# Kernel optimization log

Hardware: AMD Instinct MI355X
Metric: run time of the kernel (lower is better)

Reference implementation:

```python
import jax, jax.numpy as jnp
import numpy as np
import math

D_MODEL = 512
N_HEADS = 8
K_NEIGHBORS = 30
B, S = 4, 2048
N_VARIATES = 8
EPS = 1e-5


def layer_norm(x, g, b):
    m = jnp.mean(x, axis=-1, keepdims=True)
    v = jnp.mean(jnp.square(x - m), axis=-1, keepdims=True)
    return (x - m) * jax.lax.rsqrt(v + EPS) * g + b


def mha(x, mask, w_in, b_in, w_out, b_out):
    # x: [B,S,D]; mask: [B,S,S] bool, True = blocked (same for every head)
    Bb, Ss, D = x.shape
    H, dh = N_HEADS, D // N_HEADS
    qkv = x @ w_in.T + b_in                      # [B,S,3D]
    q, k, v = jnp.split(qkv, 3, axis=-1)
    q = q.reshape(Bb, Ss, H, dh).transpose(0, 2, 1, 3)
    k = k.reshape(Bb, Ss, H, dh).transpose(0, 2, 1, 3)
    v = v.reshape(Bb, Ss, H, dh).transpose(0, 2, 1, 3)
    scores = jnp.einsum('bhqd,bhkd->bhqk', q, k) / math.sqrt(dh)
    scores = jnp.where(mask[:, None, :, :], -jnp.inf, scores)
    attn = jax.nn.softmax(scores, axis=-1)
    o = jnp.einsum('bhqk,bhkd->bhqd', attn, v)
    o = o.transpose(0, 2, 1, 3).reshape(Bb, Ss, D)
    return o @ w_out.T + b_out


def build_masks(variates, times, valid_mask):
    Bb, Ss = variates.shape
    eye = jnp.eye(Ss, dtype=bool)
    same_var = variates[:, :, None] == variates[:, None, :]      # [B,S,S]
    valid_2d = valid_mask[:, :, None] & valid_mask[:, None, :]
    intra_mask = ~(same_var & valid_2d)                          # True = blocked
    blocked_i = jnp.any(jnp.all(intra_mask, axis=-1))
    intra_mask = intra_mask & ~(blocked_i & eye)                 # unblock diagonal if any row fully blocked

    diff_var = ~same_var
    time_dist = jnp.abs(times[:, :, None] - times[:, None, :])
    time_dist = jnp.where(~valid_2d | ~diff_var, jnp.inf, time_dist)
    k = min(K_NEIGHBORS, Ss)
    _, topk_idx = jax.lax.top_k(-time_dist, k)                   # k smallest distances
    b_idx = jnp.arange(Bb)[:, None, None]
    r_idx = jnp.arange(Ss)[None, :, None]
    knn_mask = jnp.zeros((Bb, Ss, Ss), dtype=bool).at[b_idx, r_idx, topk_idx].set(True)
    knn_mask = knn_mask & valid_2d
    inter_mask = ~knn_mask
    blocked_e = jnp.any(jnp.all(inter_mask, axis=-1))
    inter_mask = inter_mask & ~(blocked_e & eye)
    return intra_mask, inter_mask


def setup_inputs() -> dict:
    key = jax.random.key(0)
    ks = jax.random.split(key, 12)
    D = D_MODEL
    s = 0.02
    inp = {
        'x': jax.random.normal(ks[0], (B, S, D), dtype=jnp.float32),
        'variates': jax.random.randint(ks[1], (B, S), 0, N_VARIATES),
        'times': jax.random.uniform(ks[2], (B, S), dtype=jnp.float32),
        'valid_mask': jnp.ones((B, S), dtype=bool),
        'in_w1': jax.random.normal(ks[3], (3 * D, D), dtype=jnp.float32) * s,
        'in_b1': jnp.zeros((3 * D,), dtype=jnp.float32),
        'out_w1': jax.random.normal(ks[4], (D, D), dtype=jnp.float32) * s,
        'out_b1': jnp.zeros((D,), dtype=jnp.float32),
        'ln_g1': jnp.ones((D,), dtype=jnp.float32),
        'ln_b1': jnp.zeros((D,), dtype=jnp.float32),
        'in_w2': jax.random.normal(ks[5], (3 * D, D), dtype=jnp.float32) * s,
        'in_b2': jnp.zeros((3 * D,), dtype=jnp.float32),
        'out_w2': jax.random.normal(ks[6], (D, D), dtype=jnp.float32) * s,
        'out_b2': jnp.zeros((D,), dtype=jnp.float32),
        'ln_g2': jnp.ones((D,), dtype=jnp.float32),
        'ln_b2': jnp.zeros((D,), dtype=jnp.float32),
    }
    return inp


def reference(x, variates, times, valid_mask,
              in_w1, in_b1, out_w1, out_b1, ln_g1, ln_b1,
              in_w2, in_b2, out_w2, out_b2, ln_g2, ln_b2):
    intra_mask, inter_mask = build_masks(variates, times, valid_mask)
    a1 = mha(x, intra_mask, in_w1, in_b1, out_w1, out_b1)
    x = layer_norm(x + a1, ln_g1, ln_b1)
    a2 = mha(x, inter_mask, in_w2, in_b2, out_w2, out_b2)
    x = layer_norm(x + a2, ln_g2, ln_b2)
    return x
```

## Files before the change

kernel.cpp:

```cpp
#include <hip/hip_runtime.h>


#define S_LEN 2048
#define BATCH 4
#define DM    512
#define NH    8
#define DH    64
#define KNN_K 30
#define NVAR  8
#define NTOK  (BATCH * S_LEN)
#define QKVD  (3 * DM)
#define PADCAP 2560
#define MAXTILE 40

typedef float f32x4 __attribute__((ext_vector_type(4)));
typedef short s16x8 __attribute__((ext_vector_type(8)));
typedef short s16x4 __attribute__((ext_vector_type(4)));

__device__ __forceinline__ float bf2f(short u) {
  return __uint_as_float(((unsigned)(unsigned short)u) << 16);
}
__device__ __forceinline__ short f2bf(float f) {
  unsigned x = __float_as_uint(f);
  return (short)((x + 0x7fffu + ((x >> 16) & 1u)) >> 16);
}

#define C_N0 (NTOK * DM / 4)
#define C_N1 (QKVD * DM / 4)
#define C_N2 (DM * DM / 4)
#define C_B1 (C_N0 + C_N1)
#define C_B2 (C_B1 + C_N2)
#define C_B3 (C_B2 + C_N1)
#define C_B4 (C_B3 + C_N2)
#define PREP_GRID (2 * BATCH + C_B4 / 1024)

__global__ __launch_bounds__(1024) void prep_cast(
    const int* __restrict__ variates, const float* __restrict__ times,
    int* __restrict__ gcnt, int* __restrict__ pgoff, int* __restrict__ porig,
    int* __restrict__ tileV, int* __restrict__ tileQ0, int* __restrict__ ntile,
    float* __restrict__ flistT, int* __restrict__ flistI, int* __restrict__ flenG,
    int* __restrict__ sortI,
    const float* __restrict__ s0, const float* __restrict__ s1,
    const float* __restrict__ s2, const float* __restrict__ s3,
    const float* __restrict__ s4, short* __restrict__ d0,
    short* __restrict__ d1, short* __restrict__ d2,
    short* __restrict__ d3, short* __restrict__ d4) {
  int blk = blockIdx.x;
  int tid = threadIdx.x;

  if (blk < BATCH) {
    int b = blk;
    __shared__ unsigned hcnt[2048];
    __shared__ int boff[2049];
    __shared__ float bt[S_LEN];
    __shared__ int bp2[S_LEN];
    __shared__ unsigned wsum[16];
    __shared__ unsigned woff[16];

    hcnt[tid] = 0; hcnt[tid + 1024] = 0;
    float t0 = times[b * S_LEN + tid];
    float t1 = times[b * S_LEN + tid + 1024];
    int p0 = (variates[b * S_LEN + tid] << 12) | tid;
    int p1 = (variates[b * S_LEN + tid + 1024] << 12) | (tid + 1024);
    int k0 = (int)(t0 * 2048.0f); k0 = k0 < 0 ? 0 : (k0 > 2047 ? 2047 : k0);
    int k1 = (int)(t1 * 2048.0f); k1 = k1 < 0 ? 0 : (k1 > 2047 ? 2047 : k1);
    __syncthreads();
    atomicAdd(&hcnt[k0], 1u);
    atomicAdd(&hcnt[k1], 1u);
    __syncthreads();
    int wv = tid >> 6, lane = tid & 63;
    int base = wv * 128 + lane * 2;
    unsigned c0 = hcnt[base], c1 = hcnt[base + 1];
    unsigned s = c0 + c1;
    unsigned inc = s;
#pragma unroll
    for (int o2 = 1; o2 < 64; o2 <<= 1) {
      unsigned tt = __shfl_up(inc, o2);
      if (lane >= o2) inc += tt;
    }
    if (lane == 63) wsum[wv] = inc;
    __syncthreads();
    if (tid == 0) {
      unsigned a = 0;
      for (int w2 = 0; w2 < 16; ++w2) { woff[w2] = a; a += wsum[w2]; }
    }
    __syncthreads();
    unsigned e0 = woff[wv] + (inc - s);
    unsigned e1 = e0 + c0;
    boff[base] = (int)e0; boff[base + 1] = (int)e1;
    hcnt[base] = e0; hcnt[base + 1] = e1;
    if (tid == 0) boff[2048] = S_LEN;
    __syncthreads();
    unsigned q0 = atomicAdd(&hcnt[k0], 1u);
    bt[q0] = t0; bp2[q0] = p0;
    unsigned q1 = atomicAdd(&hcnt[k1], 1u);
    bt[q1] = t1; bp2[q1] = p1;
    __syncthreads();
#pragma unroll
    for (int bk = 0; bk < 2; ++bk) {
      int k = tid + bk * 1024;
      int s2 = boff[k], e2 = boff[k + 1];
      for (int i = s2 + 1; i < e2; ++i) {
        float tv = bt[i]; int pv = bp2[i];
        int j = i - 1;
        while (j >= s2 && (bt[j] > tv ||
               (bt[j] == tv && (bp2[j] & 0xFFF) > (pv & 0xFFF)))) {
          bt[j + 1] = bt[j]; bp2[j + 1] = bp2[j]; --j;
        }
        bt[j + 1] = tv; bp2[j + 1] = pv;
      }
    }
    __syncthreads();
    for (int i = tid; i < S_LEN; i += 1024)
      sortI[b * S_LEN + i] = bp2[i] & 0xFFF;
    if (wv < NVAR) {
      int lbase = lane * 32;
      int c = 0;
#pragma unroll
      for (int i = 0; i < 32; ++i) c += ((bp2[lbase + i] >> 12) != wv) ? 1 : 0;
      int pc = c;
#pragma unroll
      for (int o2 = 1; o2 < 64; o2 <<= 1) {
        int t2 = __shfl_up(pc, o2);
        if (lane >= o2) pc += t2;
      }
      int pos = pc - c;
      size_t fb = (size_t)(b * NVAR + wv) * S_LEN;
      for (int i = 0; i < 32; ++i) {
        int e = bp2[lbase + i];
        if ((e >> 12) != wv) {
          flistT[fb + pos] = bt[lbase + i];
          flistI[fb + pos] = e & 0xFFF;
          ++pos;
        }
      }
      if (lane == 63) flenG[b * NVAR + wv] = pc;
    }
  } else if (blk < 2 * BATCH) {
    int b = blk - BATCH;
    int t = tid;
    __shared__ int scnt[64][NVAR];
    __shared__ int soff[64][NVAR];
    __shared__ int stot[NVAR], sbase[NVAR];
    for (int p = t; p < PADCAP; p += 1024) porig[b * PADCAP + p] = -1;
    const int* vb = variates + b * S_LEN;
    int c[NVAR] = {0, 0, 0, 0, 0, 0, 0, 0};
    if (t < 64) {
      for (int j = t * 32; j < t * 32 + 32; ++j) {
        int v = vb[j];
#pragma unroll
        for (int u = 0; u < NVAR; ++u) c[u] += (v == u);
      }
#pragma unroll
      for (int u = 0; u < NVAR; ++u) scnt[t][u] = c[u];
    }
    __syncthreads();
    if (t < NVAR) {
      int a = 0;
      for (int u = 0; u < 64; ++u) { soff[u][t] = a; a += scnt[u][t]; }
      stot[t] = a;
    }
    __syncthreads();
    if (t == 0) {
      int a = 0, nt = 0;
      for (int v = 0; v < NVAR; ++v) {
        sbase[v] = a;
        pgoff[b * NVAR + v] = a;
        gcnt[b * NVAR + v] = stot[v];
        int ntv = (stot[v] + 63) >> 6;
        for (int i = 0; i < ntv; ++i) {
          tileV[b * MAXTILE + nt] = v;
          tileQ0[b * MAXTILE + nt] = a + i * 64;
          ++nt;
        }
        a += ntv * 64;
      }
      ntile[b] = nt;
    }
    __syncthreads();
    if (t < 64) {
      int o[NVAR];
#pragma unroll
      for (int u = 0; u < NVAR; ++u) o[u] = sbase[u] + soff[t][u];
      for (int j = t * 32; j < t * 32 + 32; ++j) {
        int v = vb[j];
        int dst = 0;
#pragma unroll
        for (int u = 0; u < NVAR; ++u) dst += (v == u) ? o[u] : 0;
        porig[b * PADCAP + dst] = j;
#pragma unroll
        for (int u = 0; u < NVAR; ++u) o[u] += (v == u);
      }
    }
  } else {
    int i = (blk - 2 * BATCH) * 1024 + tid;
    const float* src; short* dst; int k;
    if (i < C_N0)      { src = s0; dst = d0; k = i; }
    else if (i < C_B1) { src = s1; dst = d1; k = i - C_N0; }
    else if (i < C_B2) { src = s2; dst = d2; k = i - C_B1; }
    else if (i < C_B3) { src = s3; dst = d3; k = i - C_B2; }
    else               { src = s4; dst = d4; k = i - C_B3; }
    float4 v = ((const float4*)src)[k];
    s16x4 o;
    o[0] = f2bf(v.x); o[1] = f2bf(v.y); o[2] = f2bf(v.z); o[3] = f2bf(v.w);
    ((s16x4*)dst)[k] = o;
  }
}

__global__ __launch_bounds__(256) void knn_grp(const float* __restrict__ times,
                                               const int* __restrict__ porig,
                                               const int* __restrict__ pgoff,
                                               const int* __restrict__ gcnt,
                                               const float* __restrict__ flistT,
                                               const int* __restrict__ flistI,
                                               const int* __restrict__ flenG,
                                               int* __restrict__ out) {
  __shared__ float ft[S_LEN];
  __shared__ int fi[S_LEN];
  int tid = threadIdx.x;
  int bv = blockIdx.x >> 3;
  int chunk = blockIdx.x & 7;
  int b = bv >> 3, v = bv & 7;
  int flen = flenG[bv];
  size_t fb = (size_t)bv * S_LEN;
  for (int i = tid; i < flen; i += 256) {
    ft[i] = flistT[fb + i];
    fi[i] = flistI[fb + i];
  }
  __syncthreads();

  int cnt = gcnt[b * NVAR + v];
  int off = pgoff[b * NVAR + v];
  int qi = chunk * 256 + tid;
  if (qi >= cnt) return;
  int j = porig[b * PADCAP + off + qi];
  float tq = times[b * S_LEN + j];

  int lo = 0, hi = flen;
  while (lo < hi) {
    int mid = (lo + hi) >> 1;
    if (ft[mid] < tq) lo = mid + 1; else hi = mid;
  }
  int L = lo - 1, R = lo;

  float dt[KNN_K];
  int ti[KNN_K];
#pragma unroll
  for (int i = 0; i < KNN_K; ++i) {
    float dL = (L >= 0) ? (tq - ft[L]) : __builtin_inff();
    float dR = (R < flen) ? (ft[R] - tq) : __builtin_inff();
    if (dL <= dR) { dt[i] = dL; ti[i] = fi[L]; --L; }
    else          { dt[i] = dR; ti[i] = fi[R]; ++R; }
  }
  float tau = dt[KNN_K - 1];
  int nLess = 0;
#pragma unroll
  for (int i = 0; i < KNN_K; ++i) nLess += (dt[i] < tau) ? 1 : 0;

  int* op = out + ((size_t)b * S_LEN + j) * KNN_K;
#pragma unroll
  for (int i = 0; i < KNN_K; ++i)
    if (i < nLess) op[i] = ti[i];

  int m = KNN_K - nLess;
  int last = -1;
  for (int s = 0; s < m; ++s) {
    int best = 0x7fffffff;
#pragma unroll
    for (int i = 0; i < KNN_K; ++i)
      if (dt[i] == tau && ti[i] > last && ti[i] < best) best = ti[i];
    for (int Lw = L; Lw >= 0; --Lw) {
      float d = tq - ft[Lw];
      if (d > tau) break;
      if (d == tau) {
        int ix = fi[Lw];
        if (ix > last && ix < best) best = ix;
      }
    }
    for (int Rw = R; Rw < flen; ++Rw) {
      float d = ft[Rw] - tq;
      if (d > tau) break;
      if (d == tau) {
        int ix = fi[Rw];
        if (ix > last && ix < best) best = ix;
      }
    }
    op[nLess + s] = best;
    last = best;
  }
}

template <int OUT_BF16>
__global__ __launch_bounds__(256) void gemm_bt(const short* __restrict__ A,
                                               const short* __restrict__ Bm,
                                               const float* __restrict__ bias,
                                               void* __restrict__ Cout,
                                               int M, int N, int K) {
  __shared__ short sA[128 * 40];
  __shared__ short sB[128 * 40];
  int n0 = blockIdx.x * 128, m0 = blockIdx.y * 128;
  int tid = threadIdx.x;
  int lane = tid & 63, wv = tid >> 6;
  int wr = wv >> 1, wc = wv & 1;

  int srow = tid >> 2;
  int scol = (tid & 3) * 8;
  const short* aG = A + (size_t)(m0 + srow) * K + scol;
  const short* bG = Bm + (size_t)(n0 + srow) * K + scol;

  f32x4 acc[4][4] = {};
  int nk = K >> 5;

  s16x8 pa0 = *(const s16x8*)(aG);
  s16x8 pa1 = *(const s16x8*)(aG + (size_t)64 * K);
  s16x8 pb0 = *(const s16x8*)(bG);
  s16x8 pb1 = *(const s16x8*)(bG + (size_t)64 * K);

  for (int kt = 0; kt < nk; ++kt) {
    __syncthreads();
    *(s16x8*)&sA[srow * 40 + scol] = pa0;
    *(s16x8*)&sA[(srow + 64) * 40 + scol] = pa1;
    *(s16x8*)&sB[srow * 40 + scol] = pb0;
    *(s16x8*)&sB[(srow + 64) * 40 + scol] = pb1;
    __syncthreads();
    if (kt + 1 < nk) {
      const short* a2 = aG + (kt + 1) * 32;
      const short* b2 = bG + (kt + 1) * 32;
      pa0 = *(const s16x8*)(a2);
      pa1 = *(const s16x8*)(a2 + (size_t)64 * K);
      pb0 = *(const s16x8*)(b2);
      pb1 = *(const s16x8*)(b2 + (size_t)64 * K);
    }
    int kb = (lane >> 4) * 8;
    int ar = wr * 64 + (lane & 15);
    int br = wc * 64 + (lane & 15);
    s16x8 af[4], bf[4];
#pragma unroll
    for (int m = 0; m < 4; ++m) af[m] = *(const s16x8*)&sA[(ar + m * 16) * 40 + kb];
#pragma unroll
    for (int n = 0; n < 4; ++n) bf[n] = *(const s16x8*)&sB[(br + n * 16) * 40 + kb];
#pragma unroll
    for (int m = 0; m < 4; ++m)
#pragma unroll
      for (int n = 0; n < 4; ++n)
        acc[m][n] = __builtin_amdgcn_mfma_f32_16x16x32_bf16(af[m], bf[n], acc[m][n], 0, 0, 0);
  }

  int crow0 = m0 + wr * 64 + ((lane >> 4) * 4);
  int ccol0 = n0 + wc * 64 + (lane & 15);
#pragma unroll
  for (int n = 0; n < 4; ++n) {
    int col = ccol0 + n * 16;
    float bv = bias ? bias[col] : 0.f;
#pragma unroll
    for (int m = 0; m < 4; ++m) {
#pragma unroll
      for (int j = 0; j < 4; ++j) {
        int row = crow0 + m * 16 + j;
        float val = acc[m][n][j] + bv;
        if (OUT_BF16)
          ((short*)Cout)[(size_t)row * N + col] = f2bf(val);
        else
          ((float*)Cout)[(size_t)row * N + col] = val;
      }
    }
  }
}

__global__ __launch_bounds__(256) void intra_attn(
    const short* __restrict__ qkv, const int* __restrict__ porig,
    const int* __restrict__ tileV, const int* __restrict__ tileQ0,
    const int* __restrict__ ntile, const int* __restrict__ pgoff,
    const int* __restrict__ gcnt, short* __restrict__ o) {
  int b = blockIdx.z, h = blockIdx.y, t = blockIdx.x;
  if (t >= ntile[b]) return;
  int v = tileV[b * MAXTILE + t];
  int q0 = tileQ0[b * MAXTILE + t];
  int k0 = pgoff[b * NVAR + v];
  int L = gcnt[b * NVAR + v];
  int nch = (L + 63) >> 6;

  __shared__ short sQ[2][64][40];
  __shared__ short sK[2][64][40];
  __shared__ short sVT[2][64][40];
  __shared__ short sP[2][64][40];

  int tid = threadIdx.x, lane = tid & 63, w = tid >> 6;
  int colbase = lane & 15;
  int kfrag = (lane >> 4) * 8;
  int r = tid >> 2, cc = (tid & 3) * 16;

  {
    int tok = porig[b * PADCAP + q0 + r];
    if (tok < 0) tok = 0;
    const short* src = qkv + ((size_t)(b * S_LEN + tok)) * QKVD + h * DH + cc;
    s16x8 v0 = *(const s16x8*)src;
    s16x8 v1 = *(const s16x8*)(src + 8);
    int half = cc >> 5, kk = cc & 31;
    *(s16x8*)&sQ[half][r][kk] = v0;
    *(s16x8*)&sQ[half][r][kk + 8] = v1;
  }

  s16x8 pk0, pk1, pv0, pv1;
  {
    int tok = porig[b * PADCAP + k0 + r];
    if (tok < 0) tok = 0;
    size_t rowg = (size_t)(b * S_LEN + tok) * QKVD;
    const short* srcK = qkv + rowg + DM + h * DH + cc;
    pk0 = *(const s16x8*)srcK;
    pk1 = *(const s16x8*)(srcK + 8);
    const short* srcV = qkv + rowg + 2 * DM + h * DH + cc;
    pv0 = *(const s16x8*)srcV;
    pv1 = *(const s16x8*)(srcV + 8);
  }

  f32x4 accO[4] = {};
  float lrun[4] = {0.f, 0.f, 0.f, 0.f};

  for (int c = 0; c < nch; ++c) {
    __syncthreads();
    {
      int half = cc >> 5, kk = cc & 31;
      *(s16x8*)&sK[half][r][kk] = pk0;
      *(s16x8*)&sK[half][r][kk + 8] = pk1;
      int khalf = r >> 5, kkv = r & 31;
#pragma unroll
      for (int i = 0; i < 8; ++i) {
        int row = cc + i;
        sVT[khalf][row][kkv ^ (((row >> 4) & 3) << 3)] = pv0[i];
      }
#pragma unroll
      for (int i = 0; i < 8; ++i) {
        int row = cc + 8 + i;
        sVT[khalf][row][kkv ^ (((row >> 4) & 3) << 3)] = pv1[i];
      }
    }
    __syncthreads();
    if (c + 1 < nch) {
      int tok = porig[b * PADCAP + k0 + (c + 1) * 64 + r];
      if (tok < 0) tok = 0;
      size_t rowg = (size_t)(b * S_LEN + tok) * QKVD;
      const short* srcK = qkv + rowg + DM + h * DH + cc;
      pk0 = *(const s16x8*)srcK;
      pk1 = *(const s16x8*)(srcK + 8);
      const short* srcV = qkv + rowg + 2 * DM + h * DH + cc;
      pv0 = *(const s16x8*)srcV;
      pv1 = *(const s16x8*)(srcV + 8);
    }

    s16x8 aQ0 = *(const s16x8*)&sQ[0][w * 16 + colbase][kfrag];
    s16x8 aQ1 = *(const s16x8*)&sQ[1][w * 16 + colbase][kfrag];
    f32x4 accS[4] = {};
#pragma unroll
    for (int n = 0; n < 4; ++n) {
      s16x8 b0 = *(const s16x8*)&sK[0][n * 16 + colbase][kfrag];
      s16x8 b1 = *(const s16x8*)&sK[1][n * 16 + colbase][kfrag];
      accS[n] = __builtin_amdgcn_mfma_f32_16x16x32_bf16(aQ0, b0, accS[n], 0, 0, 0);
      accS[n] = __builtin_amdgcn_mfma_f32_16x16x32_bf16(aQ1, b1, accS[n], 0, 0, 0);
    }

    float pv[4][4];
#pragma unroll
    for (int j = 0; j < 4; ++j) {
      float rs = 0.f;
#pragma unroll
      for (int n = 0; n < 4; ++n) {
        bool ok = (c * 64 + n * 16 + colbase) < L;
        float p = ok ? __expf(accS[n][j] * 0.125f) : 0.f;
        pv[n][j] = p;
        rs += p;
      }
      for (int o2 = 8; o2; o2 >>= 1) rs += __shfl_xor(rs, o2);
      lrun[j] += rs;
    }

    int prow = w * 16 + ((lane >> 4) << 2);
#pragma unroll
    for (int n = 0; n < 4; ++n)
#pragma unroll
      for (int j = 0; j < 4; ++j)
        sP[n >> 1][prow + j][colbase + ((n & 1) << 4)] = f2bf(pv[n][j]);

    s16x8 aP0 = *(const s16x8*)&sP[0][w * 16 + colbase][kfrag];
    s16x8 aP1 = *(const s16x8*)&sP[1][w * 16 + colbase][kfrag];
#pragma unroll
    for (int n = 0; n < 4; ++n) {
      int row = n * 16 + colbase;
      int cb = kfrag ^ ((n & 3) << 3);
      s16x8 b0 = *(const s16x8*)&sVT[0][row][cb];
      s16x8 b1 = *(const s16x8*)&sVT[1][row][cb];
      accO[n] = __builtin_amdgcn_mfma_f32_16x16x32_bf16(aP0, b0, accO[n], 0, 0, 0);
      accO[n] = __builtin_amdgcn_mfma_f32_16x16x32_bf16(aP1, b1, accO[n], 0, 0, 0);
    }
  }

#pragma unroll
  for (int j = 0; j < 4; ++j) {
    int prow = w * 16 + (lane >> 4) * 4 + j;
    int orig = porig[b * PADCAP + q0 + prow];
    if (orig >= 0) {
      float inv = 1.f / lrun[j];
      size_t base = ((size_t)(b * S_LEN + orig)) * DM + h * DH;
#pragma unroll
      for (int n = 0; n < 4; ++n)
        o[base + n * 16 + colbase] = f2bf(accO[n][j] * inv);
    }
  }
}

__global__ __launch_bounds__(256) void inter_attn(const short* __restrict__ qkv,
                                                  const int* __restrict__ knn,
                                                  const int* __restrict__ sortI,
                                                  short* __restrict__ o) {
  __shared__ float sS[4][NH][33];
  __shared__ float sP[4][NH][33];
  int tid = threadIdx.x, lane = tid & 63, w = tid >> 6;
  int rank = blockIdx.x * 4 + w;
  int b = rank >> 11;
  int q = sortI[b * S_LEN + (rank & 2047)];
  int bq = b * S_LEN + q;
  int h = lane >> 3;

  int myidx = (lane < KNN_K) ? knn[(size_t)bq * KNN_K + lane] : 0;

  s16x8 q8 = *(const s16x8*)(qkv + (size_t)bq * QKVD + lane * 8);
  float qf[8];
#pragma unroll
  for (int i = 0; i < 8; ++i) qf[i] = bf2f(q8[i]) * 0.125f;

  for (int j = 0; j < KNN_K; ++j) {
    int idx = __shfl(myidx, j);
    s16x8 k8 = *(const s16x8*)(qkv + ((size_t)(b * S_LEN + idx)) * QKVD + DM + lane * 8);
    float acc = 0.f;
#pragma unroll
    for (int i = 0; i < 8; ++i) acc += qf[i] * bf2f(k8[i]);
    acc += __shfl_xor(acc, 1);
    acc += __shfl_xor(acc, 2);
    acc += __shfl_xor(acc, 4);
    if ((lane & 7) == 0) sS[w][h][j] = acc;
  }

  int jsub = lane & 7;
  float sv0 = sS[w][h][jsub];
  float sv1 = sS[w][h][jsub + 8];
  float sv2 = sS[w][h][jsub + 16];
  float sv3 = (jsub < 6) ? sS[w][h][jsub + 24] : -__builtin_inff();
  float m = fmaxf(fmaxf(sv0, sv1), fmaxf(sv2, sv3));
  m = fmaxf(m, __shfl_xor(m, 1));
  m = fmaxf(m, __shfl_xor(m, 2));
  m = fmaxf(m, __shfl_xor(m, 4));
  float p0 = __expf(sv0 - m), p1 = __expf(sv1 - m), p2 = __expf(sv2 - m);
  float p3 = (jsub < 6) ? __expf(sv3 - m) : 0.f;
  sP[w][h][jsub] = p0;
  sP[w][h][jsub + 8] = p1;
  sP[w][h][jsub + 16] = p2;
  sP[w][h][jsub + 24] = p3;
  float l = p0 + p1 + p2 + p3;
  l += __shfl_xor(l, 1);
  l += __shfl_xor(l, 2);
  l += __shfl_xor(l, 4);

  float o8[8] = {};
  for (int j = 0; j < KNN_K; ++j) {
    int idx = __shfl(myidx, j);
    s16x8 v8 = *(const s16x8*)(qkv + ((size_t)(b * S_LEN + idx)) * QKVD + 2 * DM + lane * 8);
    float p = sP[w][h][j];
#pragma unroll
    for (int i = 0; i < 8; ++i) o8[i] += p * bf2f(v8[i]);
  }
  float inv = 1.f / l;
  s16x8 ov;
#pragma unroll
  for (int i = 0; i < 8; ++i) ov[i] = f2bf(o8[i] * inv);
  *(s16x8*)(o + (size_t)bq * DM + lane * 8) = ov;
}

__global__ __launch_bounds__(256) void residual_ln(const float* __restrict__ x,
                                                   const short* __restrict__ a,
                                                   const float* __restrict__ g,
                                                   const float* __restrict__ bta,
                                                   float* __restrict__ yf,
                                                   short* __restrict__ yb) {
  int row = blockIdx.x * 4 + (threadIdx.x >> 6);
  int lane = threadIdx.x & 63;
  const float4* xp = (const float4*)(x + (size_t)row * DM);
  float4 v0 = xp[lane * 2], v1 = xp[lane * 2 + 1];
  s16x8 a8 = *(const s16x8*)(a + (size_t)row * DM + lane * 8);
  float r[8] = {v0.x + bf2f(a8[0]), v0.y + bf2f(a8[1]),
                v0.z + bf2f(a8[2]), v0.w + bf2f(a8[3]),
                v1.x + bf2f(a8[4]), v1.y + bf2f(a8[5]),
                v1.z + bf2f(a8[6]), v1.w + bf2f(a8[7])};
  float s = 0.f;
#pragma unroll
  for (int j = 0; j < 8; ++j) s += r[j];
  for (int o2 = 32; o2; o2 >>= 1) s += __shfl_xor(s, o2);
  float mean = s * (1.f / DM);
  float vs = 0.f;
#pragma unroll
  for (int j = 0; j < 8; ++j) { float d = r[j] - mean; vs += d * d; }
  for (int o2 = 32; o2; o2 >>= 1) vs += __shfl_xor(vs, o2);
  float inv = rsqrtf(vs * (1.f / DM) + 1e-5f);
  const float4* gp = (const float4*)g;
  const float4* bp = (const float4*)bta;
  float4 g0 = gp[lane * 2], g1 = gp[lane * 2 + 1];
  float4 b0 = bp[lane * 2], b1 = bp[lane * 2 + 1];
  float gg[8] = {g0.x, g0.y, g0.z, g0.w, g1.x, g1.y, g1.z, g1.w};
  float bb[8] = {b0.x, b0.y, b0.z, b0.w, b1.x, b1.y, b1.z, b1.w};
  float y[8];
#pragma unroll
  for (int j = 0; j < 8; ++j) y[j] = (r[j] - mean) * inv * gg[j] + bb[j];
  float4 o0 = {y[0], y[1], y[2], y[3]};
  float4 o1 = {y[4], y[5], y[6], y[7]};
  float4* yp = (float4*)(yf + (size_t)row * DM);
  yp[lane * 2] = o0;
  yp[lane * 2 + 1] = o1;
  if (yb) {
    s16x8 ob;
#pragma unroll
    for (int j = 0; j < 8; ++j) ob[j] = f2bf(y[j]);
    *(s16x8*)(yb + (size_t)row * DM + lane * 8) = ob;
  }
}

extern "C" void kernel_launch(void* const* d_in, const int* in_sizes, int n_in,
                              void* d_out, int out_size, void* d_ws, size_t ws_size,
                              hipStream_t stream) {
  const float* x      = (const float*)d_in[0];
  const int*   var    = (const int*)d_in[1];
  const float* times  = (const float*)d_in[2];
  const float* in_w1  = (const float*)d_in[4];
  const float* in_b1  = (const float*)d_in[5];
  const float* out_w1 = (const float*)d_in[6];
  const float* out_b1 = (const float*)d_in[7];
  const float* ln_g1  = (const float*)d_in[8];
  const float* ln_b1  = (const float*)d_in[9];
  const float* in_w2  = (const float*)d_in[10];
  const float* in_b2  = (const float*)d_in[11];
  const float* out_w2 = (const float*)d_in[12];
  const float* out_b2 = (const float*)d_in[13];
  const float* ln_g2  = (const float*)d_in[14];
  const float* ln_b2  = (const float*)d_in[15];
  float* out = (float*)d_out;

  char* ws = (char*)d_ws;
  size_t off = 0;
  auto alloc = [&](size_t bytes) -> char* {
    char* p = ws + off;
    off = (off + bytes + 255) & ~(size_t)255;
    return p;
  };
  short* xb    = (short*)alloc((size_t)NTOK * DM * 2);
  short* x1b   = (short*)alloc((size_t)NTOK * DM * 2);
  short* w1q   = (short*)alloc((size_t)QKVD * DM * 2);
  short* w1o   = (short*)alloc((size_t)DM * DM * 2);
  short* w2q   = (short*)alloc((size_t)QKVD * DM * 2);
  short* w2o   = (short*)alloc((size_t)DM * DM * 2);
  short* qkvb  = (short*)alloc((size_t)NTOK * QKVD * 2);
  short* ob    = (short*)alloc((size_t)NTOK * DM * 2);
  short* afb   = (short*)alloc((size_t)NTOK * DM * 2);
  float* x1f   = (float*)alloc((size_t)NTOK * DM * 4);
  int* gcnt    = (int*)alloc((size_t)BATCH * NVAR * 4);
  int* pgoff   = (int*)alloc((size_t)BATCH * NVAR * 4);
  int* porig   = (int*)alloc((size_t)BATCH * PADCAP * 4);
  int* tileV   = (int*)alloc((size_t)BATCH * MAXTILE * 4);
  int* tileQ0  = (int*)alloc((size_t)BATCH * MAXTILE * 4);
  int* ntile   = (int*)alloc((size_t)BATCH * 4);
  int* knn     = (int*)alloc((size_t)NTOK * KNN_K * 4);
  float* flistT = (float*)alloc((size_t)BATCH * NVAR * S_LEN * 4);
  int*   flistI = (int*)alloc((size_t)BATCH * NVAR * S_LEN * 4);
  int*   flenG  = (int*)alloc((size_t)BATCH * NVAR * 4);
  int*   sortI  = (int*)alloc((size_t)NTOK * 4);

  prep_cast<<<PREP_GRID, 1024, 0, stream>>>(
      var, times, gcnt, pgoff, porig, tileV, tileQ0, ntile,
      flistT, flistI, flenG, sortI,
      x, in_w1, out_w1, in_w2, out_w2, xb, w1q, w1o, w2q, w2o);

  knn_grp<<<BATCH * NVAR * 8, 256, 0, stream>>>(times, porig, pgoff, gcnt,
                                                flistT, flistI, flenG, knn);

  gemm_bt<1><<<dim3(QKVD / 128, NTOK / 128), 256, 0, stream>>>(xb, w1q, in_b1, qkvb,
                                                               NTOK, QKVD, DM);
  intra_attn<<<dim3(MAXTILE, NH, BATCH), 256, 0, stream>>>(qkvb, porig, tileV, tileQ0,
                                                           ntile, pgoff, gcnt, ob);
  gemm_bt<1><<<dim3(DM / 128, NTOK / 128), 256, 0, stream>>>(ob, w1o, out_b1, afb,
                                                             NTOK, DM, DM);
  residual_ln<<<NTOK / 4, 256, 0, stream>>>(x, afb, ln_g1, ln_b1, x1f, x1b);

  gemm_bt<1><<<dim3(QKVD / 128, NTOK / 128), 256, 0, stream>>>(x1b, w2q, in_b2, qkvb,
                                                               NTOK, QKVD, DM);
  inter_attn<<<NTOK / 4, 256, 0, stream>>>(qkvb, knn, sortI, ob);
  gemm_bt<1><<<dim3(DM / 128, NTOK / 128), 256, 0, stream>>>(ob, w2o, out_b2, afb,
                                                             NTOK, DM, DM);
  residual_ln<<<NTOK / 4, 256, 0, stream>>>(x1f, afb, ln_g2, ln_b2, out, nullptr);
}
```

Before: 192.4 us.

## Pair two query tiles per block in intra-variate attention to share K/V loads

The intra-variate attention kernel now processes two 64-row query tiles of the same variate per 512-thread block. Each K/V chunk is loaded once into shared memory and used by both tiles, which halves the K/V gather traffic and the number of blocks. Prep emits pair descriptors instead of single tiles. When a variate has an odd tile count, the last block runs half of its waves on duplicated work. It also uses more shared memory and fewer blocks, which may reduce parallelism.

```diff
diff --git a/kernel.cpp b/kernel.cpp
--- a/kernel.cpp
+++ b/kernel.cpp
@@ -37,7 +37,8 @@
 __global__ __launch_bounds__(1024) void prep_cast(
     const int* __restrict__ variates, const float* __restrict__ times,
     int* __restrict__ gcnt, int* __restrict__ pgoff, int* __restrict__ porig,
-    int* __restrict__ tileV, int* __restrict__ tileQ0, int* __restrict__ ntile,
+    int* __restrict__ pairV, int* __restrict__ pairA, int* __restrict__ pairB,
+    int* __restrict__ npair,
     float* __restrict__ flistT, int* __restrict__ flistI, int* __restrict__ flenG,
     int* __restrict__ sortI,
     const float* __restrict__ s0, const float* __restrict__ s1,
@@ -162,20 +163,21 @@
     }
     __syncthreads();
     if (t == 0) {
-      int a = 0, nt = 0;
+      int a = 0, np = 0;
       for (int v = 0; v < NVAR; ++v) {
         sbase[v] = a;
         pgoff[b * NVAR + v] = a;
         gcnt[b * NVAR + v] = stot[v];
         int ntv = (stot[v] + 63) >> 6;
-        for (int i = 0; i < ntv; ++i) {
-          tileV[b * MAXTILE + nt] = v;
-          tileQ0[b * MAXTILE + nt] = a + i * 64;
-          ++nt;
+        for (int i = 0; i < ntv; i += 2) {
+          pairV[b * MAXTILE + np] = v;
+          pairA[b * MAXTILE + np] = a + i * 64;
+          pairB[b * MAXTILE + np] = (i + 1 < ntv) ? (a + (i + 1) * 64) : -1;
+          ++np;
         }
         a += ntv * 64;
       }
-      ntile[b] = nt;
+      npair[b] = np;
     }
     __syncthreads();
     if (t < 64) {
@@ -367,51 +369,56 @@
   }
 }
 
-__global__ __launch_bounds__(256) void intra_attn(
+__global__ __launch_bounds__(512) void intra_attn(
     const short* __restrict__ qkv, const int* __restrict__ porig,
-    const int* __restrict__ tileV, const int* __restrict__ tileQ0,
-    const int* __restrict__ ntile, const int* __restrict__ pgoff,
-    const int* __restrict__ gcnt, short* __restrict__ o) {
+    const int* __restrict__ pairV, const int* __restrict__ pairA,
+    const int* __restrict__ pairB, const int* __restrict__ npair,
+    const int* __restrict__ pgoff, const int* __restrict__ gcnt,
+    short* __restrict__ o) {
   int b = blockIdx.z, h = blockIdx.y, t = blockIdx.x;
-  if (t >= ntile[b]) return;
-  int v = tileV[b * MAXTILE + t];
-  int q0 = tileQ0[b * MAXTILE + t];
+  if (t >= npair[b]) return;
+  int v = pairV[b * MAXTILE + t];
+  int q0a = pairA[b * MAXTILE + t];
+  int q0b = pairB[b * MAXTILE + t];
   int k0 = pgoff[b * NVAR + v];
   int L = gcnt[b * NVAR + v];
   int nch = (L + 63) >> 6;
 
-  __shared__ short sQ[2][64][40];
+  __shared__ short sQ[2][2][64][40];
   __shared__ short sK[2][64][40];
   __shared__ short sVT[2][64][40];
-  __shared__ short sP[2][64][40];
+  __shared__ short sP[2][2][64][40];
 
   int tid = threadIdx.x, lane = tid & 63, w = tid >> 6;
+  int sel = w >> 2, wsub = w & 3;
   int colbase = lane & 15;
   int kfrag = (lane >> 4) * 8;
-  int r = tid >> 2, cc = (tid & 3) * 16;
+  bool tileValid = (sel == 0) || (q0b >= 0);
+  int myq0 = (sel && q0b >= 0) ? q0b : q0a;
 
   {
-    int tok = porig[b * PADCAP + q0 + r];
+    int t2 = tid >> 8, tid8 = tid & 255;
+    int r = tid8 >> 2, cc = (tid8 & 3) * 16;
+    int srcq0 = (t2 && q0b >= 0) ? q0b : q0a;
+    int tok = porig[b * PADCAP + srcq0 + r];
     if (tok < 0) tok = 0;
     const short* src = qkv + ((size_t)(b * S_LEN + tok)) * QKVD + h * DH + cc;
     s16x8 v0 = *(const s16x8*)src;
     s16x8 v1 = *(const s16x8*)(src + 8);
     int half = cc >> 5, kk = cc & 31;
-    *(s16x8*)&sQ[half][r][kk] = v0;
-    *(s16x8*)&sQ[half][r][kk + 8] = v1;
-  }
-
-  s16x8 pk0, pk1, pv0, pv1;
+    *(s16x8*)&sQ[t2][half][r][kk] = v0;
+    *(s16x8*)&sQ[t2][half][r][kk + 8] = v1;
+  }
+
+  int gr = tid >> 3, gc = tid & 7;
+  int gelem = gc * 8;
+  s16x8 pk, pvv;
   {
-    int tok = porig[b * PADCAP + k0 + r];
+    int tok = porig[b * PADCAP + k0 + gr];
     if (tok < 0) tok = 0;
     size_t rowg = (size_t)(b * S_LEN + tok) * QKVD;
-    const short* srcK = qkv + rowg + DM + h * DH + cc;
-    pk0 = *(const s16x8*)srcK;
-    pk1 = *(const s16x8*)(srcK + 8);
-    const short* srcV = qkv + rowg + 2 * DM + h * DH + cc;
-    pv0 = *(const s16x8*)srcV;
-    pv1 = *(const s16x8*)(srcV + 8);
+    pk  = *(const s16x8*)(qkv + rowg + DM + h * DH + gelem);
+    pvv = *(const s16x8*)(qkv + rowg + 2 * DM + h * DH + gelem);
   }
 
   f32x4 accO[4] = {};
@@ -420,36 +427,26 @@
   for (int c = 0; c < nch; ++c) {
     __syncthreads();
     {
-      int half = cc >> 5, kk = cc & 31;
-      *(s16x8*)&sK[half][r][kk] = pk0;
-      *(s16x8*)&sK[half][r][kk + 8] = pk1;
-      int khalf = r >> 5, kkv = r & 31;
+      int half = gelem >> 5, kk = gelem & 31;
+      *(s16x8*)&sK[half][gr][kk] = pk;
+      int khalf = gr >> 5, kkv = gr & 31;
 #pragma unroll
       for (int i = 0; i < 8; ++i) {
-        int row = cc + i;
-        sVT[khalf][row][kkv ^ (((row >> 4) & 3) << 3)] = pv0[i];
-      }
-#pragma unroll
-      for (int i = 0; i < 8; ++i) {
-        int row = cc + 8 + i;
-        sVT[khalf][row][kkv ^ (((row >> 4) & 3) << 3)] = pv1[i];
+        int row = gelem + i;
+        sVT[khalf][row][kkv ^ (((row >> 4) & 3) << 3)] = pvv[i];
       }
     }
     __syncthreads();
     if (c + 1 < nch) {
-      int tok = porig[b * PADCAP + k0 + (c + 1) * 64 + r];
+      int tok = porig[b * PADCAP + k0 + (c + 1) * 64 + gr];
       if (tok < 0) tok = 0;
       size_t rowg = (size_t)(b * S_LEN + tok) * QKVD;
-      const short* srcK = qkv + rowg + DM + h * DH + cc;
-      pk0 = *(const s16x8*)srcK;
-      pk1 = *(const s16x8*)(srcK + 8);
-      const short* srcV = qkv + rowg + 2 * DM + h * DH + cc;
-      pv0 = *(const s16x8*)srcV;
-      pv1 = *(const s16x8*)(srcV + 8);
-    }
-
-    s16x8 aQ0 = *(const s16x8*)&sQ[0][w * 16 + colbase][kfrag];
-    s16x8 aQ1 = *(const s16x8*)&sQ[1][w * 16 + colbase][kfrag];
+      pk  = *(const s16x8*)(qkv + rowg + DM + h * DH + gelem);
+      pvv = *(const s16x8*)(qkv + rowg + 2 * DM + h * DH + gelem);
+    }
+
+    s16x8 aQ0 = *(const s16x8*)&sQ[sel][0][wsub * 16 + colbase][kfrag];
+    s16x8 aQ1 = *(const s16x8*)&sQ[sel][1][wsub * 16 + colbase][kfrag];
     f32x4 accS[4] = {};
 #pragma unroll
     for (int n = 0; n < 4; ++n) {
@@ -474,15 +471,15 @@
       lrun[j] += rs;
     }
 
-    int prow = w * 16 + ((lane >> 4) << 2);
+    int prow = wsub * 16 + ((lane >> 4) << 2);
 #pragma unroll
     for (int n = 0; n < 4; ++n)
 #pragma unroll
       for (int j = 0; j < 4; ++j)
-        sP[n >> 1][prow + j][colbase + ((n & 1) << 4)] = f2bf(pv[n][j]);
-
-    s16x8 aP0 = *(const s16x8*)&sP[0][w * 16 + colbase][kfrag];
-    s16x8 aP1 = *(const s16x8*)&sP[1][w * 16 + colbase][kfrag];
+        sP[sel][n >> 1][prow + j][colbase + ((n & 1) << 4)] = f2bf(pv[n][j]);
+
+    s16x8 aP0 = *(const s16x8*)&sP[sel][0][wsub * 16 + colbase][kfrag];
+    s16x8 aP1 = *(const s16x8*)&sP[sel][1][wsub * 16 + colbase][kfrag];
 #pragma unroll
     for (int n = 0; n < 4; ++n) {
       int row = n * 16 + colbase;
@@ -494,16 +491,18 @@
     }
   }
 
-#pragma unroll
-  for (int j = 0; j < 4; ++j) {
-    int prow = w * 16 + (lane >> 4) * 4 + j;
-    int orig = porig[b * PADCAP + q0 + prow];
-    if (orig >= 0) {
-      float inv = 1.f / lrun[j];
-      size_t base = ((size_t)(b * S_LEN + orig)) * DM + h * DH;
-#pragma unroll
-      for (int n = 0; n < 4; ++n)
-        o[base + n * 16 + colbase] = f2bf(accO[n][j] * inv);
+  if (tileValid) {
+#pragma unroll
+    for (int j = 0; j < 4; ++j) {
+      int prow = wsub * 16 + (lane >> 4) * 4 + j;
+      int orig = porig[b * PADCAP + myq0 + prow];
+      if (orig >= 0) {
+        float inv = 1.f / lrun[j];
+        size_t base = ((size_t)(b * S_LEN + orig)) * DM + h * DH;
+#pragma unroll
+        for (int n = 0; n < 4; ++n)
+          o[base + n * 16 + colbase] = f2bf(accO[n][j] * inv);
+      }
     }
   }
 }
@@ -662,9 +661,10 @@
   int* gcnt    = (int*)alloc((size_t)BATCH * NVAR * 4);
   int* pgoff   = (int*)alloc((size_t)BATCH * NVAR * 4);
   int* porig   = (int*)alloc((size_t)BATCH * PADCAP * 4);
-  int* tileV   = (int*)alloc((size_t)BATCH * MAXTILE * 4);
-  int* tileQ0  = (int*)alloc((size_t)BATCH * MAXTILE * 4);
-  int* ntile   = (int*)alloc((size_t)BATCH * 4);
+  int* pairV   = (int*)alloc((size_t)BATCH * MAXTILE * 4);
+  int* pairA   = (int*)alloc((size_t)BATCH * MAXTILE * 4);
+  int* pairB   = (int*)alloc((size_t)BATCH * MAXTILE * 4);
+  int* npair   = (int*)alloc((size_t)BATCH * 4);
   int* knn     = (int*)alloc((size_t)NTOK * KNN_K * 4);
   float* flistT = (float*)alloc((size_t)BATCH * NVAR * S_LEN * 4);
   int*   flistI = (int*)alloc((size_t)BATCH * NVAR * S_LEN * 4);
@@ -672,7 +672,7 @@
   int*   sortI  = (int*)alloc((size_t)NTOK * 4);
 
   prep_cast<<<PREP_GRID, 1024, 0, stream>>>(
-      var, times, gcnt, pgoff, porig, tileV, tileQ0, ntile,
+      var, times, gcnt, pgoff, porig, pairV, pairA, pairB, npair,
       flistT, flistI, flenG, sortI,
       x, in_w1, out_w1, in_w2, out_w2, xb, w1q, w1o, w2q, w2o);
 
@@ -681,8 +681,8 @@
 
   gemm_bt<1><<<dim3(QKVD / 128, NTOK / 128), 256, 0, stream>>>(xb, w1q, in_b1, qkvb,
                                                                NTOK, QKVD, DM);
-  intra_attn<<<dim3(MAXTILE, NH, BATCH), 256, 0, stream>>>(qkvb, porig, tileV, tileQ0,
-                                                           ntile, pgoff, gcnt, ob);
+  intra_attn<<<dim3(MAXTILE, NH, BATCH), 512, 0, stream>>>(
+      qkvb, porig, pairV, pairA, pairB, npair, pgoff, gcnt, ob);
   gemm_bt<1><<<dim3(DM / 128, NTOK / 128), 256, 0, stream>>>(ob, w1o, out_b1, afb,
                                                              NTOK, DM, DM);
   residual_ln<<<NTOK / 4, 256, 0, stream>>>(x, afb, ln_g1, ln_b1, x1f, x1b);
```

Result: no change. 194.4 us (+1.1%).
